# Optimization experiments

Hardware: AMD Instinct MI355X
Metric: run time of the kernel (lower is better)

Reference implementation:

```python
import jax, jax.numpy as jnp
import numpy as np

B, N, D, H = 4, 4096, 1024, 16
HD = D // H


def setup_inputs() -> dict:
    key = jax.random.key(0)
    k_x, k_qkv, k_proj, k_b = jax.random.split(key, 4)
    x = jax.random.normal(k_x, (B, N, D), dtype=jnp.float32)
    # torch nn.Linear weights: (out_features, in_features)
    w_qkv = jax.random.normal(k_qkv, (3 * D, D), dtype=jnp.float32) * (D ** -0.5)
    w_proj = jax.random.normal(k_proj, (D, D), dtype=jnp.float32) * (D ** -0.5)
    b_proj = jax.random.normal(k_b, (D,), dtype=jnp.float32) * 0.01
    return {"x": x, "w_qkv": w_qkv, "w_proj": w_proj, "b_proj": b_proj}


def reference(x, w_qkv, w_proj, b_proj):
    b, n, d = x.shape
    # qkv projection (no bias, qkv_bias=False)
    qkv = x @ w_qkv.T                       # (b, n, 3d)
    qkv = qkv.reshape(b, n, 3, H, HD)
    q, k, v = qkv[:, :, 0], qkv[:, :, 1], qkv[:, :, 2]   # each (b, n, H, HD)
    # Faithful to source: q @ k.transpose(-2,-1) with q,k of shape (b,n,H,HD)
    # -> per-token (H,H) attention across heads, softmax over last (head) axis.
    scale = HD ** -0.5
    attn = jnp.einsum('bnhd,bngd->bnhg', q, k) * scale   # (b, n, H, H)
    attn = jax.nn.softmax(attn, axis=-1)
    o = jnp.einsum('bnhg,bngd->bnhd', attn, v)           # (b, n, H, HD)
    # source: transpose(1,2).reshape(b,n,d) (contiguous copy then reshape)
    o = jnp.swapaxes(o, 1, 2).reshape(b, n, d)
    return o @ w_proj.T + b_proj
```

## Files before the change

kernel.cpp:

```cpp
#include <hip/hip_runtime.h>
#include <hip/hip_bf16.h>
#include <cstdint>
#include <cstddef>

#define NB      4
#define NSEQ    4096
#define DM      1024
#define NTOK    16384
#define QKV_N   3072

typedef __attribute__((ext_vector_type(8))) short short8_t;
typedef __attribute__((ext_vector_type(4))) float f32x4;

static __device__ __forceinline__ unsigned short f2bf(float f) {
    unsigned u = __builtin_bit_cast(unsigned, f);
    u += 0x7fffu + ((u >> 16) & 1u);
    return (unsigned short)(u >> 16);
}

static __device__ __forceinline__ void async16(const void* g, void* l) {
    __builtin_amdgcn_global_load_lds(
        (const __attribute__((address_space(1))) void*)g,
        (__attribute__((address_space(3))) void*)l, 16, 0, 0);
}

__global__ void cvt_all(const float* __restrict__ x,
                        const float* __restrict__ wqkv,
                        const float* __restrict__ wproj,
                        unsigned short* __restrict__ xb,
                        unsigned short* __restrict__ wqkvb,
                        unsigned short* __restrict__ wprojb)
{
    int i = blockIdx.x * blockDim.x + threadIdx.x;
    const float* src; unsigned short* dst; int off;
    if (i < 4194304)      { src = x;     dst = xb;     off = i; }
    else if (i < 4980736) { src = wqkv;  dst = wqkvb;  off = i - 4194304; }
    else                  { src = wproj; dst = wprojb; off = i - 4980736; }
    float4 f = ((const float4*)src)[off];
    unsigned lo = (unsigned)f2bf(f.x) | ((unsigned)f2bf(f.y) << 16);
    unsigned hi = (unsigned)f2bf(f.z) | ((unsigned)f2bf(f.w) << 16);
    ((uint2*)dst)[off] = make_uint2(lo, hi);
}

template <bool BF16_OUT, bool BIAS>
__global__ __launch_bounds__(256)
void gemm_bt(const unsigned short* __restrict__ A,
             const unsigned short* __restrict__ Bm,
             void* __restrict__ Cv,
             const float* __restrict__ bias,
             int M, int N, int K)
{
    __shared__ alignas(16) unsigned short As[128 * 32];
    __shared__ alignas(16) unsigned short Bs[128 * 32];
    const int t    = threadIdx.x;
    const int lane = t & 63;
    const int quad = lane >> 4;
    const int r16  = lane & 15;
    const int wave = t >> 6;
    const int wm   = (wave >> 1) * 64;
    const int wn   = (wave & 1) * 64;
    const int m0   = blockIdx.y * 128;
    const int n0   = blockIdx.x * 128;

    const int c0 = t, c1 = t + 256;
    const unsigned short* gA0 = A  + (size_t)(m0 + (c0 >> 2)) * K + (c0 & 3) * 8;
    const unsigned short* gA1 = A  + (size_t)(m0 + (c1 >> 2)) * K + (c1 & 3) * 8;
    const unsigned short* gB0 = Bm + (size_t)(n0 + (c0 >> 2)) * K + (c0 & 3) * 8;
    const unsigned short* gB1 = Bm + (size_t)(n0 + (c1 >> 2)) * K + (c1 & 3) * 8;

    f32x4 acc[4][4] = {};

    for (int k0 = 0; k0 < K; k0 += 32) {
        async16(gA0 + k0, As + c0 * 8);
        async16(gA1 + k0, As + c1 * 8);
        async16(gB0 + k0, Bs + c0 * 8);
        async16(gB1 + k0, Bs + c1 * 8);
        __syncthreads();

        short8_t a[4], b[4];
        #pragma unroll
        for (int i = 0; i < 4; ++i)
            a[i] = *(const short8_t*)(As + (wm + i * 16 + r16) * 32 + quad * 8);
        #pragma unroll
        for (int j = 0; j < 4; ++j)
            b[j] = *(const short8_t*)(Bs + (wn + j * 16 + r16) * 32 + quad * 8);
        #pragma unroll
        for (int i = 0; i < 4; ++i)
            #pragma unroll
            for (int j = 0; j < 4; ++j)
                acc[i][j] = __builtin_amdgcn_mfma_f32_16x16x32_bf16(
                    a[i], b[j], acc[i][j], 0, 0, 0);
        __syncthreads();
    }

    #pragma unroll
    for (int i = 0; i < 4; ++i) {
        #pragma unroll
        for (int j = 0; j < 4; ++j) {
            const int col = n0 + wn + j * 16 + r16;
            float bv = 0.f;
            if constexpr (BIAS) bv = bias[col];
            #pragma unroll
            for (int r = 0; r < 4; ++r) {
                const int row = m0 + wm + i * 16 + quad * 4 + r;
                float v = acc[i][j][r] + bv;
                if constexpr (BF16_OUT)
                    ((unsigned short*)Cv)[(size_t)row * N + col] = f2bf(v);
                else
                    ((float*)Cv)[(size_t)row * N + col] = v;
            }
        }
    }
}

__global__ __launch_bounds__(256)
void attn_kernel(const unsigned short* __restrict__ qkv,
                 unsigned short* __restrict__ operm)
{
    __shared__ alignas(16) unsigned short s_qkv[4][QKV_N];
    __shared__ alignas(16) unsigned short s_p[4][256];
    __shared__ alignas(16) unsigned short s_o[4][16 * 72];
    const int t     = threadIdx.x;
    const int lane  = t & 63;
    const int wave  = t >> 6;
    const int quad  = lane >> 4;
    const int r16   = lane & 15;
    const int token = blockIdx.x * 4 + wave;

    {
        const unsigned short* src = qkv + (size_t)token * QKV_N;
        #pragma unroll
        for (int i = 0; i < 6; ++i)
            async16(src + i * 512 + lane * 8, &s_qkv[wave][i * 512 + lane * 8]);
    }
    __syncthreads();

    const unsigned short* q  = &s_qkv[wave][0];
    const unsigned short* kk = q + 1024;
    const unsigned short* vv = q + 2048;

    f32x4 s = {};
    #pragma unroll
    for (int c = 0; c < 64; c += 32) {
        short8_t aq = *(const short8_t*)(q  + r16 * 64 + c + quad * 8);
        short8_t bk = *(const short8_t*)(kk + r16 * 64 + c + quad * 8);
        s = __builtin_amdgcn_mfma_f32_16x16x32_bf16(aq, bk, s, 0, 0, 0);
    }

    #pragma unroll
    for (int r = 0; r < 4; ++r) {
        float x = s[r] * 0.125f;
        float m = x;
        #pragma unroll
        for (int o = 1; o < 16; o <<= 1) m = fmaxf(m, __shfl_xor(m, o));
        float e = __expf(x - m);
        float su = e;
        #pragma unroll
        for (int o = 1; o < 16; o <<= 1) su += __shfl_xor(su, o);
        s_p[wave][(quad * 4 + r) * 16 + r16] = f2bf(e * __builtin_amdgcn_rcpf(su));
    }
    __syncthreads();

    short8_t pa = {};
    if (quad < 2) pa = *(const short8_t*)(&s_p[wave][r16 * 16 + quad * 8]);

    f32x4 o[4];
    #pragma unroll
    for (int j = 0; j < 4; ++j) {
        short8_t vb = {};
        if (quad < 2) {
            #pragma unroll
            for (int e = 0; e < 8; ++e)
                vb[e] = (short)vv[(quad * 8 + e) * 64 + j * 16 + r16];
        }
        f32x4 z = {};
        o[j] = __builtin_amdgcn_mfma_f32_16x16x32_bf16(pa, vb, z, 0, 0, 0);
    }

    #pragma unroll
    for (int j = 0; j < 4; ++j)
        #pragma unroll
        for (int r = 0; r < 4; ++r)
            s_o[wave][(quad * 4 + r) * 72 + j * 16 + r16] = f2bf(o[j][r]);
    __syncthreads();

    const int b    = token >> 12;
    const int npos = token & 4095;
    const size_t base = (size_t)b * (NSEQ * DM)
                      + (size_t)(npos >> 4) * 1024
                      + (size_t)(npos & 15) * 64;
    #pragma unroll
    for (int c = lane; c < 128; c += 64) {
        const int h = c >> 3, part = c & 7;
        int4 val = *(const int4*)(&s_o[wave][h * 72 + part * 8]);
        *(int4*)(operm + base + (size_t)h * (256 * 1024) + part * 8) = val;
    }
}

extern "C" void kernel_launch(void* const* d_in, const int* in_sizes, int n_in,
                              void* d_out, int out_size, void* d_ws, size_t ws_size,
                              hipStream_t stream)
{
    const float* x      = (const float*)d_in[0];
    const float* w_qkv  = (const float*)d_in[1];
    const float* w_proj = (const float*)d_in[2];
    const float* b_proj = (const float*)d_in[3];
    float* out = (float*)d_out;

    unsigned short* xb     = (unsigned short*)d_ws;
    unsigned short* wqkvb  = xb     + (size_t)16777216;
    unsigned short* wprojb = wqkvb  + (size_t)3145728;
    unsigned short* qkvb   = wprojb + (size_t)1048576;
    unsigned short* opermb = qkvb   + (size_t)50331648;

    cvt_all<<<20480, 256, 0, stream>>>(x, w_qkv, w_proj, xb, wqkvb, wprojb);

    dim3 g1(QKV_N / 128, NTOK / 128);
    gemm_bt<true, false><<<g1, 256, 0, stream>>>(xb, wqkvb, qkvb, nullptr,
                                                 NTOK, QKV_N, DM);

    attn_kernel<<<NTOK / 4, 256, 0, stream>>>(qkvb, opermb);

    dim3 g2(DM / 128, NTOK / 128);
    gemm_bt<false, true><<<g2, 256, 0, stream>>>(opermb, wprojb, out, b_proj,
                                                 NTOK, DM, DM);
}
```

Baseline: 353.2 us.

## Swizzle GEMM LDS tiles and process two K slices per barrier

The GEMM now loads two 32-wide K slices into separate LDS buffers before a single barrier, halving the number of synchronizations per K step. It also applies an XOR swizzle on 16-byte chunks, keyed on the row index, when placing global data into LDS. The fragment reads use the matching swizzle to reduce LDS bank conflicts. LDS usage doubles, and there is still no overlap of loads with compute.

```diff
diff --git a/kernel.cpp b/kernel.cpp
--- a/kernel.cpp
+++ b/kernel.cpp
@@ -50,8 +50,8 @@
              const float* __restrict__ bias,
              int M, int N, int K)
 {
-    __shared__ alignas(16) unsigned short As[128 * 32];
-    __shared__ alignas(16) unsigned short Bs[128 * 32];
+    __shared__ alignas(16) unsigned short As[2][128 * 32];
+    __shared__ alignas(16) unsigned short Bs[2][128 * 32];
     const int t    = threadIdx.x;
     const int lane = t & 63;
     const int quad = lane >> 4;
@@ -63,33 +63,45 @@
     const int n0   = blockIdx.x * 128;
 
     const int c0 = t, c1 = t + 256;
-    const unsigned short* gA0 = A  + (size_t)(m0 + (c0 >> 2)) * K + (c0 & 3) * 8;
-    const unsigned short* gA1 = A  + (size_t)(m0 + (c1 >> 2)) * K + (c1 & 3) * 8;
-    const unsigned short* gB0 = Bm + (size_t)(n0 + (c0 >> 2)) * K + (c0 & 3) * 8;
-    const unsigned short* gB1 = Bm + (size_t)(n0 + (c1 >> 2)) * K + (c1 & 3) * 8;
+    const int ra0 = c0 >> 2, ra1 = c1 >> 2;
+    const int f0 = (ra0 & 3) ^ ((ra0 >> 2) & 3);
+    const int f1 = (ra1 & 3) ^ ((ra1 >> 2) & 3);
+    const unsigned short* gA0 = A  + (size_t)(m0 + ra0) * K + (((c0 & 3) ^ f0)) * 8;
+    const unsigned short* gA1 = A  + (size_t)(m0 + ra1) * K + (((c1 & 3) ^ f1)) * 8;
+    const unsigned short* gB0 = Bm + (size_t)(n0 + ra0) * K + (((c0 & 3) ^ f0)) * 8;
+    const unsigned short* gB1 = Bm + (size_t)(n0 + ra1) * K + (((c1 & 3) ^ f1)) * 8;
+
+    const int qa = ((quad ^ ((r16 & 3) ^ ((r16 >> 2) & 3))) * 8);
 
     f32x4 acc[4][4] = {};
 
-    for (int k0 = 0; k0 < K; k0 += 32) {
-        async16(gA0 + k0, As + c0 * 8);
-        async16(gA1 + k0, As + c1 * 8);
-        async16(gB0 + k0, Bs + c0 * 8);
-        async16(gB1 + k0, Bs + c1 * 8);
+    for (int k0 = 0; k0 < K; k0 += 64) {
+        #pragma unroll
+        for (int s = 0; s < 2; ++s) {
+            const int ks = k0 + s * 32;
+            async16(gA0 + ks, &As[s][c0 * 8]);
+            async16(gA1 + ks, &As[s][c1 * 8]);
+            async16(gB0 + ks, &Bs[s][c0 * 8]);
+            async16(gB1 + ks, &Bs[s][c1 * 8]);
+        }
         __syncthreads();
 
-        short8_t a[4], b[4];
-        #pragma unroll
-        for (int i = 0; i < 4; ++i)
-            a[i] = *(const short8_t*)(As + (wm + i * 16 + r16) * 32 + quad * 8);
-        #pragma unroll
-        for (int j = 0; j < 4; ++j)
-            b[j] = *(const short8_t*)(Bs + (wn + j * 16 + r16) * 32 + quad * 8);
-        #pragma unroll
-        for (int i = 0; i < 4; ++i)
+        #pragma unroll
+        for (int s = 0; s < 2; ++s) {
+            short8_t a[4], b[4];
+            #pragma unroll
+            for (int i = 0; i < 4; ++i)
+                a[i] = *(const short8_t*)(&As[s][(wm + i * 16 + r16) * 32 + qa]);
             #pragma unroll
             for (int j = 0; j < 4; ++j)
-                acc[i][j] = __builtin_amdgcn_mfma_f32_16x16x32_bf16(
-                    a[i], b[j], acc[i][j], 0, 0, 0);
+                b[j] = *(const short8_t*)(&Bs[s][(wn + j * 16 + r16) * 32 + qa]);
+            #pragma unroll
+            for (int i = 0; i < 4; ++i)
+                #pragma unroll
+                for (int j = 0; j < 4; ++j)
+                    acc[i][j] = __builtin_amdgcn_mfma_f32_16x16x32_bf16(
+                        a[i], b[j], acc[i][j], 0, 0, 0);
+        }
         __syncthreads();
     }
 
```

Measured after the change: 326.9 us. 1.08x faster.

## Double-buffer LDS tiles in the bf16 GEMM to overlap loads with MFMA

Applied to the files above, without the earlier changes.

Splits the shared-memory A and B tiles of the GEMM into two buffers. The async global-to-LDS copy for the next K-slice is issued before the MFMA work on the current slice, so load latency can hide behind compute. The K loop is unrolled by two to alternate buffers. In exchange it doubles LDS use per block, which may lower occupancy, and it assumes the number of K-steps is even.

```diff
diff --git a/kernel.cpp b/kernel.cpp
--- a/kernel.cpp
+++ b/kernel.cpp
@@ -50,8 +50,8 @@
              const float* __restrict__ bias,
              int M, int N, int K)
 {
-    __shared__ alignas(16) unsigned short As[128 * 32];
-    __shared__ alignas(16) unsigned short Bs[128 * 32];
+    __shared__ alignas(16) unsigned short As[2][128 * 32];
+    __shared__ alignas(16) unsigned short Bs[2][128 * 32];
     const int t    = threadIdx.x;
     const int lane = t & 63;
     const int quad = lane >> 4;
@@ -70,27 +70,38 @@
 
     f32x4 acc[4][4] = {};
 
-    for (int k0 = 0; k0 < K; k0 += 32) {
-        async16(gA0 + k0, As + c0 * 8);
-        async16(gA1 + k0, As + c1 * 8);
-        async16(gB0 + k0, Bs + c0 * 8);
-        async16(gB1 + k0, Bs + c1 * 8);
-        __syncthreads();
-
-        short8_t a[4], b[4];
+    auto stage = [&](int s, int b) {
+        const int ks = s * 32;
+        async16(gA0 + ks, &As[b][c0 * 8]);
+        async16(gA1 + ks, &As[b][c1 * 8]);
+        async16(gB0 + ks, &Bs[b][c0 * 8]);
+        async16(gB1 + ks, &Bs[b][c1 * 8]);
+    };
+    auto compute = [&](int b) {
+        short8_t a[4], bb[4];
         #pragma unroll
         for (int i = 0; i < 4; ++i)
-            a[i] = *(const short8_t*)(As + (wm + i * 16 + r16) * 32 + quad * 8);
+            a[i] = *(const short8_t*)(&As[b][(wm + i * 16 + r16) * 32 + quad * 8]);
         #pragma unroll
         for (int j = 0; j < 4; ++j)
-            b[j] = *(const short8_t*)(Bs + (wn + j * 16 + r16) * 32 + quad * 8);
+            bb[j] = *(const short8_t*)(&Bs[b][(wn + j * 16 + r16) * 32 + quad * 8]);
         #pragma unroll
         for (int i = 0; i < 4; ++i)
             #pragma unroll
             for (int j = 0; j < 4; ++j)
                 acc[i][j] = __builtin_amdgcn_mfma_f32_16x16x32_bf16(
-                    a[i], b[j], acc[i][j], 0, 0, 0);
+                    a[i], bb[j], acc[i][j], 0, 0, 0);
+    };
+
+    const int S = K >> 5;
+    stage(0, 0);
+    for (int s = 0; s < S; s += 2) {
         __syncthreads();
+        stage(s + 1, 1);
+        compute(0);
+        __syncthreads();
+        if (s + 2 < S) stage(s + 2, 0);
+        compute(1);
     }
 
     #pragma unroll
```

New measurement: 346.8 us. About the same (-1.8%).
